# Kernel tuning notes

Hardware: AMD Instinct MI355X
Metric: run time of the kernel (lower is better)

The kernel has to match this reference:

```python
import jax, jax.numpy as jnp
import numpy as np

ALPHA = 0.2  # leaky-relu negative slope


def setup_inputs() -> dict:
    key = jax.random.key(0)
    k1, k2, k3, k4 = jax.random.split(key, 4)
    bs, L, D, Fin, Fout = 4, 20000, 16, 128, 128
    x = jax.random.normal(k1, (bs, L, Fin), dtype=jnp.float32)
    adj = jax.random.randint(k2, (bs, L, D), 0, L, dtype=jnp.int64)
    # xavier_normal-ish init for W [Fin, Fout] and a [2*Fout, 1]
    W = jax.random.normal(k3, (Fin, Fout), dtype=jnp.float32) * (1.414 * np.sqrt(2.0 / (Fin + Fout))).astype(np.float32)
    a = jax.random.normal(k4, (2 * Fout, 1), dtype=jnp.float32) * (1.414 * np.sqrt(2.0 / (2 * Fout + 1))).astype(np.float32)
    return {"x": x, "adj": adj, "W": W, "a": a}


def reference(x, adj, W, a):
    Fout = W.shape[1]
    # gather fixed-degree neighbor features: [bs, L, D, Fin]
    nbr = jax.vmap(lambda xb, ab: xb[ab])(x, adj)
    h = jnp.matmul(nbr, W)  # [bs, L, D, Fout]
    # a is applied to cat([h_neighbor, h_center]); split it instead of concatenating
    a1 = a[:Fout, 0]
    a2 = a[Fout:, 0]
    # h[:, :, 0, :] is the center node (first neighbor slot, repeat_interleave in torch)
    e = jnp.einsum('bldf,f->bld', h, a1) + jnp.einsum('blf,f->bl', h[:, :, 0, :], a2)[..., None]
    attn = jax.nn.softmax(jax.nn.leaky_relu(e, ALPHA), axis=-1)  # softmax over D
    out = jnp.einsum('bld,bldf->blf', attn, h)  # weighted aggregate [bs, L, Fout]
    return jax.nn.elu(out)  # concat=True branch
```

## Files before the change

kernel.cpp:

```cpp
#include <hip/hip_runtime.h>
#include <hip/hip_bf16.h>

#define LSEQ 20000
#define DEG  16
#define F    128
#define ALPHA 0.2f

typedef __bf16 bf16x8 __attribute__((ext_vector_type(8)));
typedef float  f32x4  __attribute__((ext_vector_type(4)));

__global__ __launch_bounds__(256) void gat_wt(const float* __restrict__ W,
                                              __hip_bfloat16* __restrict__ wt)
{
    for (int i = blockIdx.x * 256 + threadIdx.x; i < F * F; i += 16 * 256) {
        const int k = i >> 7, n = i & (F - 1);
        wt[n * F + k] = __float2bfloat16(W[i]);
    }
}

__global__ __launch_bounds__(256) void gat_gemm(const float* __restrict__ x,
                                                const __hip_bfloat16* __restrict__ wt,
                                                const float* __restrict__ a,
                                                __hip_bfloat16* __restrict__ y16,
                                                float* __restrict__ s1,
                                                float* __restrict__ s2)
{
    const int lane = threadIdx.x & 63;
    const int wv   = (blockIdx.x * 256 + threadIdx.x) >> 6;
    const int row0 = wv * 32;
    const int m    = lane & 15;
    const int q    = lane >> 4;

    bf16x8 afr[2][4];
    #pragma unroll
    for (int h = 0; h < 2; ++h) {
        const float* xr = x + (size_t)(row0 + h * 16 + m) * F + q * 8;
        #pragma unroll
        for (int kt = 0; kt < 4; ++kt) {
            const float4 q0 = *reinterpret_cast<const float4*>(xr + kt * 32);
            const float4 q1 = *reinterpret_cast<const float4*>(xr + kt * 32 + 4);
            bf16x8 f;
            f[0] = (__bf16)q0.x; f[1] = (__bf16)q0.y; f[2] = (__bf16)q0.z; f[3] = (__bf16)q0.w;
            f[4] = (__bf16)q1.x; f[5] = (__bf16)q1.y; f[6] = (__bf16)q1.z; f[7] = (__bf16)q1.w;
            afr[h][kt] = f;
        }
    }

    float p1[2][4] = {{0.f,0.f,0.f,0.f},{0.f,0.f,0.f,0.f}};
    float p2[2][4] = {{0.f,0.f,0.f,0.f},{0.f,0.f,0.f,0.f}};
    const __hip_bfloat16* wb = wt + (size_t)m * F + q * 8;

    #pragma unroll 2
    for (int ct = 0; ct < 8; ++ct) {
        union { uint4 u; bf16x8 v; } b[4];
        #pragma unroll
        for (int kt = 0; kt < 4; ++kt)
            b[kt].u = *reinterpret_cast<const uint4*>(wb + (size_t)ct * 16 * F + kt * 32);

        const int col = ct * 16 + m;
        const float a1v = a[col];
        const float a2v = a[F + col];

        #pragma unroll
        for (int h = 0; h < 2; ++h) {
            f32x4 acc = {0.f, 0.f, 0.f, 0.f};
            #pragma unroll
            for (int kt = 0; kt < 4; ++kt)
                acc = __builtin_amdgcn_mfma_f32_16x16x32_bf16(afr[h][kt], b[kt].v, acc, 0, 0, 0);
            #pragma unroll
            for (int r = 0; r < 4; ++r) {
                const int row = row0 + h * 16 + q * 4 + r;
                y16[(size_t)row * F + col] = __float2bfloat16(acc[r]);
                p1[h][r] = fmaf(acc[r], a1v, p1[h][r]);
                p2[h][r] = fmaf(acc[r], a2v, p2[h][r]);
            }
        }
    }

    #pragma unroll
    for (int h = 0; h < 2; ++h) {
        #pragma unroll
        for (int r = 0; r < 4; ++r) {
            #pragma unroll
            for (int off = 1; off < 16; off <<= 1) {
                p1[h][r] += __shfl_xor(p1[h][r], off);
                p2[h][r] += __shfl_xor(p2[h][r], off);
            }
        }
    }
    if (m == 0) {
        #pragma unroll
        for (int h = 0; h < 2; ++h) {
            #pragma unroll
            for (int r = 0; r < 4; ++r) {
                s1[row0 + h * 16 + q * 4 + r] = p1[h][r];
                s2[row0 + h * 16 + q * 4 + r] = p2[h][r];
            }
        }
    }
}

__global__ __launch_bounds__(256) void gat_attn(const int* __restrict__ adj,
                                                const __hip_bfloat16* __restrict__ y16,
                                                const float* __restrict__ s1,
                                                const float* __restrict__ s2,
                                                float* __restrict__ out)
{
    const int lane = threadIdx.x & 63;
    const int wid  = threadIdx.x >> 6;
    const int gl   = blockIdx.x * 4 + wid;
    const int b    = gl / LSEQ;
    const int base = b * LSEQ;

    const int* adjp = adj + (size_t)gl * DEG;
    int av = (lane < DEG) ? adjp[lane] : 0;

    float sv = (lane < DEG) ? s1[base + av] : 0.f;
    const int a0 = __builtin_amdgcn_readlane(av, 0);
    const float e = sv + s2[base + a0];
    const float t = e > 0.f ? e : ALPHA * e;

    float m = t;
    #pragma unroll
    for (int off = 8; off; off >>= 1) m = fmaxf(m, __shfl_xor(m, off));
    float w = (lane < DEG) ? __expf(t - m) : 0.f;
    float p = w;
    #pragma unroll
    for (int off = 8; off; off >>= 1) p += __shfl_xor(p, off);
    const float attn = w / p;

    unsigned int v[DEG];
    #pragma unroll
    for (int d = 0; d < DEG; ++d) {
        const int nb = __builtin_amdgcn_readlane(av, d);
        const unsigned int* row =
            reinterpret_cast<const unsigned int*>(y16 + ((size_t)(base + nb) << 7));
        v[d] = row[lane];
    }

    float accx = 0.f, accy = 0.f;
    #pragma unroll
    for (int d = 0; d < DEG; ++d) {
        const float ad = __uint_as_float(
            __builtin_amdgcn_readlane(__float_as_uint(attn), d));
        accx = fmaf(ad, __uint_as_float(v[d] << 16),          accx);
        accy = fmaf(ad, __uint_as_float(v[d] & 0xffff0000u),  accy);
    }
    const float ox = accx > 0.f ? accx : __expf(accx) - 1.f;
    const float oy = accy > 0.f ? accy : __expf(accy) - 1.f;
    *reinterpret_cast<float2*>(out + (size_t)gl * F + lane * 2) = make_float2(ox, oy);
}

extern "C" void kernel_launch(void* const* d_in, const int* in_sizes, int n_in,
                              void* d_out, int out_size, void* d_ws, size_t ws_size,
                              hipStream_t stream) {
    const float* x   = (const float*)d_in[0];
    const int*   adj = (const int*)d_in[1];
    const float* W   = (const float*)d_in[2];
    const float* a   = (const float*)d_in[3];
    float* out = (float*)d_out;

    const int BL = in_sizes[0] / F;

    __hip_bfloat16* y16 = (__hip_bfloat16*)d_ws;
    float* s1 = (float*)((char*)d_ws + (size_t)BL * F * sizeof(__hip_bfloat16));
    float* s2 = s1 + BL;
    __hip_bfloat16* wt = (__hip_bfloat16*)(s2 + BL);

    gat_wt  <<<16, 256, 0, stream>>>(W, wt);
    gat_gemm<<<BL / 128, 256, 0, stream>>>(x, wt, a, y16, s1, s2);
    gat_attn<<<BL / 4, 256, 0, stream>>>(adj, y16, s1, s2, out);
}
```

Before: 145.1 us.

## Precompute W·a vectors and transpose MFMA operands for packed output stores

```diff
diff --git a/kernel.cpp b/kernel.cpp
--- a/kernel.cpp
+++ b/kernel.cpp
@@ -10,93 +10,104 @@
 typedef float  f32x4  __attribute__((ext_vector_type(4)));
 
 __global__ __launch_bounds__(256) void gat_wt(const float* __restrict__ W,
-                                              __hip_bfloat16* __restrict__ wt)
+                                              const float* __restrict__ a,
+                                              __hip_bfloat16* __restrict__ wt,
+                                              float* __restrict__ wa)
 {
-    for (int i = blockIdx.x * 256 + threadIdx.x; i < F * F; i += 16 * 256) {
+    const int t = blockIdx.x * 256 + threadIdx.x;
+    for (int i = t; i < F * F; i += 16 * 256) {
         const int k = i >> 7, n = i & (F - 1);
         wt[n * F + k] = __float2bfloat16(W[i]);
+    }
+    if (blockIdx.x == 0 && threadIdx.x < F) {
+        const int k = threadIdx.x;
+        float acc1 = 0.f, acc2 = 0.f;
+        for (int n = 0; n < F; ++n) {
+            const float w = W[k * F + n];
+            acc1 = fmaf(w, a[n],     acc1);
+            acc2 = fmaf(w, a[F + n], acc2);
+        }
+        wa[k]     = acc1;
+        wa[F + k] = acc2;
     }
 }
 
 __global__ __launch_bounds__(256) void gat_gemm(const float* __restrict__ x,
                                                 const __hip_bfloat16* __restrict__ wt,
-                                                const float* __restrict__ a,
+                                                const float* __restrict__ wa,
                                                 __hip_bfloat16* __restrict__ y16,
                                                 float* __restrict__ s1,
                                                 float* __restrict__ s2)
 {
     const int lane = threadIdx.x & 63;
     const int wv   = (blockIdx.x * 256 + threadIdx.x) >> 6;
-    const int row0 = wv * 32;
+    const int i0   = wv * 16;
     const int m    = lane & 15;
     const int q    = lane >> 4;
 
-    bf16x8 afr[2][4];
+    const float* xr = x + (size_t)(i0 + m) * F + q * 8;
+    float4 xf[8];
     #pragma unroll
-    for (int h = 0; h < 2; ++h) {
-        const float* xr = x + (size_t)(row0 + h * 16 + m) * F + q * 8;
+    for (int kt = 0; kt < 4; ++kt) {
+        xf[2*kt]   = *reinterpret_cast<const float4*>(xr + kt * 32);
+        xf[2*kt+1] = *reinterpret_cast<const float4*>(xr + kt * 32 + 4);
+    }
+
+    float p1 = 0.f, p2 = 0.f;
+    {
+        const float* w1p = wa + q * 8;
+        const float* w2p = wa + F + q * 8;
         #pragma unroll
         for (int kt = 0; kt < 4; ++kt) {
-            const float4 q0 = *reinterpret_cast<const float4*>(xr + kt * 32);
-            const float4 q1 = *reinterpret_cast<const float4*>(xr + kt * 32 + 4);
-            bf16x8 f;
-            f[0] = (__bf16)q0.x; f[1] = (__bf16)q0.y; f[2] = (__bf16)q0.z; f[3] = (__bf16)q0.w;
-            f[4] = (__bf16)q1.x; f[5] = (__bf16)q1.y; f[6] = (__bf16)q1.z; f[7] = (__bf16)q1.w;
-            afr[h][kt] = f;
+            const float4 u0 = *reinterpret_cast<const float4*>(w1p + kt * 32);
+            const float4 u1 = *reinterpret_cast<const float4*>(w1p + kt * 32 + 4);
+            const float4 v0 = *reinterpret_cast<const float4*>(w2p + kt * 32);
+            const float4 v1 = *reinterpret_cast<const float4*>(w2p + kt * 32 + 4);
+            const float4 xa = xf[2*kt], xb = xf[2*kt+1];
+            p1 = fmaf(xa.x,u0.x,p1); p1 = fmaf(xa.y,u0.y,p1);
+            p1 = fmaf(xa.z,u0.z,p1); p1 = fmaf(xa.w,u0.w,p1);
+            p1 = fmaf(xb.x,u1.x,p1); p1 = fmaf(xb.y,u1.y,p1);
+            p1 = fmaf(xb.z,u1.z,p1); p1 = fmaf(xb.w,u1.w,p1);
+            p2 = fmaf(xa.x,v0.x,p2); p2 = fmaf(xa.y,v0.y,p2);
+            p2 = fmaf(xa.z,v0.z,p2); p2 = fmaf(xa.w,v0.w,p2);
+            p2 = fmaf(xb.x,v1.x,p2); p2 = fmaf(xb.y,v1.y,p2);
+            p2 = fmaf(xb.z,v1.z,p2); p2 = fmaf(xb.w,v1.w,p2);
         }
     }
+    p1 += __shfl_xor(p1, 16); p1 += __shfl_xor(p1, 32);
+    p2 += __shfl_xor(p2, 16); p2 += __shfl_xor(p2, 32);
+    if (lane < 16) {
+        s1[i0 + m] = p1;
+        s2[i0 + m] = p2;
+    }
 
-    float p1[2][4] = {{0.f,0.f,0.f,0.f},{0.f,0.f,0.f,0.f}};
-    float p2[2][4] = {{0.f,0.f,0.f,0.f},{0.f,0.f,0.f,0.f}};
-    const __hip_bfloat16* wb = wt + (size_t)m * F + q * 8;
-
-    #pragma unroll 2
-    for (int ct = 0; ct < 8; ++ct) {
-        union { uint4 u; bf16x8 v; } b[4];
-        #pragma unroll
-        for (int kt = 0; kt < 4; ++kt)
-            b[kt].u = *reinterpret_cast<const uint4*>(wb + (size_t)ct * 16 * F + kt * 32);
-
-        const int col = ct * 16 + m;
-        const float a1v = a[col];
-        const float a2v = a[F + col];
-
-        #pragma unroll
-        for (int h = 0; h < 2; ++h) {
-            f32x4 acc = {0.f, 0.f, 0.f, 0.f};
-            #pragma unroll
-            for (int kt = 0; kt < 4; ++kt)
-                acc = __builtin_amdgcn_mfma_f32_16x16x32_bf16(afr[h][kt], b[kt].v, acc, 0, 0, 0);
-            #pragma unroll
-            for (int r = 0; r < 4; ++r) {
-                const int row = row0 + h * 16 + q * 4 + r;
-                y16[(size_t)row * F + col] = __float2bfloat16(acc[r]);
-                p1[h][r] = fmaf(acc[r], a1v, p1[h][r]);
-                p2[h][r] = fmaf(acc[r], a2v, p2[h][r]);
-            }
-        }
+    bf16x8 bfr[4];
+    #pragma unroll
+    for (int kt = 0; kt < 4; ++kt) {
+        const float4 qa = xf[2*kt], qb = xf[2*kt+1];
+        bf16x8 f;
+        f[0] = (__bf16)qa.x; f[1] = (__bf16)qa.y; f[2] = (__bf16)qa.z; f[3] = (__bf16)qa.w;
+        f[4] = (__bf16)qb.x; f[5] = (__bf16)qb.y; f[6] = (__bf16)qb.z; f[7] = (__bf16)qb.w;
+        bfr[kt] = f;
     }
 
     #pragma unroll
-    for (int h = 0; h < 2; ++h) {
+    for (int ct = 0; ct < 8; ++ct) {
+        union { uint4 u; bf16x8 v; } afr[4];
+        const __hip_bfloat16* wrow = wt + (size_t)(ct * 16 + m) * F + q * 8;
         #pragma unroll
-        for (int r = 0; r < 4; ++r) {
-            #pragma unroll
-            for (int off = 1; off < 16; off <<= 1) {
-                p1[h][r] += __shfl_xor(p1[h][r], off);
-                p2[h][r] += __shfl_xor(p2[h][r], off);
-            }
-        }
-    }
-    if (m == 0) {
+        for (int kt = 0; kt < 4; ++kt)
+            afr[kt].u = *reinterpret_cast<const uint4*>(wrow + kt * 32);
+
+        f32x4 acc = {0.f, 0.f, 0.f, 0.f};
         #pragma unroll
-        for (int h = 0; h < 2; ++h) {
-            #pragma unroll
-            for (int r = 0; r < 4; ++r) {
-                s1[row0 + h * 16 + q * 4 + r] = p1[h][r];
-                s2[row0 + h * 16 + q * 4 + r] = p2[h][r];
-            }
-        }
+        for (int kt = 0; kt < 4; ++kt)
+            acc = __builtin_amdgcn_mfma_f32_16x16x32_bf16(afr[kt].v, bfr[kt], acc, 0, 0, 0);
+
+        union { uint2 u; __hip_bfloat162 h[2]; } pk;
+        pk.h[0] = __float22bfloat162_rn(make_float2(acc[0], acc[1]));
+        pk.h[1] = __float22bfloat162_rn(make_float2(acc[2], acc[3]));
+        *reinterpret_cast<uint2*>(y16 + (size_t)(i0 + m) * F + ct * 16 + q * 4) = pk.u;
     }
 }
 
@@ -166,8 +177,9 @@
     float* s1 = (float*)((char*)d_ws + (size_t)BL * F * sizeof(__hip_bfloat16));
     float* s2 = s1 + BL;
     __hip_bfloat16* wt = (__hip_bfloat16*)(s2 + BL);
+    float* wa = (float*)(wt + F * F);
 
-    gat_wt  <<<16, 256, 0, stream>>>(W, wt);
-    gat_gemm<<<BL / 128, 256, 0, stream>>>(x, wt, a, y16, s1, s2);
+    gat_wt  <<<16, 256, 0, stream>>>(W, a, wt, wa);
+    gat_gemm<<<BL / 64, 256, 0, stream>>>(x, wt, wa, y16, s1, s2);
     gat_attn<<<BL / 4, 256, 0, stream>>>(adj, y16, s1, s2, out);
 }
```

New measurement: 155.1 us. 6.9% more time.
